# Kernel optimization log

Measured on AMD Instinct MI355X. Metric: run time of the kernel, lower is better.

## Reference

```python
import jax, jax.numpy as jnp
import numpy as np

EPS = 1e-5


def bin_act(x):
    # forward of Binaryactivation: sign (STE backward handled in fwdbwd module)
    return jnp.sign(x)


def bin_conv(x, w, stride, padding):
    # per-output-filter scaling factor = mean |w| over (in, kh, kw), detached
    scale = jax.lax.stop_gradient(jnp.mean(jnp.abs(w), axis=(1, 2, 3), keepdims=True))
    bw = scale * jnp.sign(w)
    rw = jnp.clip(w, -1.0, 1.0)
    # STE blend: forward uses binary weight, backward flows through clamp(w)
    filt = jax.lax.stop_gradient(bw - rw) + rw
    return jax.lax.conv_general_dilated(
        x, filt, window_strides=(stride, stride),
        padding=[(padding, padding), (padding, padding)],
        dimension_numbers=("NCHW", "OIHW", "NCHW"))


def batchnorm(x, gamma, beta):
    # training-mode BN: biased batch stats over (N, H, W)
    mean = jnp.mean(x, axis=(0, 2, 3), keepdims=True)
    var = jnp.mean((x - mean) ** 2, axis=(0, 2, 3), keepdims=True)
    xn = (x - mean) * jax.lax.rsqrt(var + EPS)
    return xn * gamma[None, :, None, None] + beta[None, :, None, None]


def prelu(x, a):
    a = a[None, :, None, None]
    return jnp.where(x >= 0, x, a * x)


def addbias(x, b):
    return x + b[None, :, None, None]


def setup_inputs() -> dict:
    key = jax.random.key(0)
    ks = jax.random.split(key, 4)
    C = 256
    x = jax.random.normal(ks[0], (32, C, 56, 56), dtype=jnp.float32)
    # BinaryConv weights init: uniform[0, 0.001)
    w3x3 = jax.random.uniform(ks[1], (C, C, 3, 3), dtype=jnp.float32) * 0.001
    wres = jax.random.uniform(ks[2], (C, C, 1, 1), dtype=jnp.float32) * 0.001
    zeros = jnp.zeros((C,), dtype=jnp.float32)
    ones = jnp.ones((C,), dtype=jnp.float32)
    prelu_init = jnp.full((C,), 0.25, dtype=jnp.float32)
    return {
        "x": x,
        "b1_1": zeros, "w3x3": w3x3, "bn1_g": ones, "bn1_b": zeros,
        "b1_2": zeros, "prelu1_a": prelu_init, "b1_3": zeros,
        "b2_1": zeros, "wres": wres, "bn2_g": ones, "bn2_b": zeros,
        "b2_2": zeros, "prelu2_a": prelu_init, "b2_3": zeros,
    }


def reference(x, b1_1, w3x3, bn1_g, bn1_b, b1_2, prelu1_a, b1_3,
              b2_1, wres, bn2_g, bn2_b, b2_2, prelu2_a, b2_3):
    # branch 1: bias -> sign -> binary 3x3 conv -> BN -> residual add
    x1 = bin_act(addbias(x, b1_1))
    x1 = bin_conv(x1, w3x3, stride=1, padding=1)
    x1 = batchnorm(x1, bn1_g, bn1_b)
    x = x + x1
    x = addbias(x, b1_2)
    x = prelu(x, prelu1_a)
    x = addbias(x, b1_3)
    # branch 2 (in_channel == out_channel): binary 1x1 conv residual
    x2 = bin_act(addbias(x, b2_1))
    x2 = bin_conv(x2, wres, stride=1, padding=0)
    x2 = batchnorm(x2, bn2_g, bn2_b)
    x2 = x2 + x
    x2 = addbias(x2, b2_2)
    x2 = prelu(x2, prelu2_a)
    x2 = addbias(x2, b2_3)
    return x2
```

## Files before the change

### kernel.cpp

```cpp
#include <hip/hip_runtime.h>
#include <cstdint>
#include <math.h>

#define NIMG 32
#define CCH  256
#define HH_  56
#define HW   3136
#define NPIX 100352
#define NELEM 25690112

#define OFF_PW1   0u
#define OFF_PW2   73728u
#define OFF_SC1   81920u
#define OFF_SC2   82944u
#define OFF_A1    83968u
#define OFF_B1    84992u
#define OFF_A2    86016u
#define OFF_B2    87040u
#define OFF_ST    88064u
#define ST_BYTES  524288u
#define OFF_P1    612352u
#define OFF_P2    3823616u
#define OFF_S1    7034880u
#define OFF_S2    58415104u

__global__ void prep_w_k(const float* __restrict__ w3, const float* __restrict__ wr,
                         uint32_t* __restrict__ pw1, uint32_t* __restrict__ pw2,
                         float* __restrict__ sc1, float* __restrict__ sc2) {
  const int o = blockIdx.x, l = threadIdx.x;
  const float* wo = w3 + (size_t)o * 2304;
  float s = 0.f;
  for (int i = l; i < 2304; i += 64) s += fabsf(wo[i]);
  for (int m = 32; m; m >>= 1) s += __shfl_xor(s, m, 64);
  if (l == 0) sc1[o] = s / 2304.0f;
  for (int tap = 0; tap < 9; ++tap) {
    int dh = tap / 3, dw = tap % 3;
    for (int jp = 0; jp < 4; ++jp) {
      int ci = jp * 64 + l;
      float wv = wo[(size_t)ci * 9 + dh * 3 + dw];
      unsigned long long m = __ballot(wv >= 0.0f);
      if (l == 0) {
        pw1[(size_t)(o * 9 + tap) * 8 + jp * 2 + 0] = (uint32_t)m;
        pw1[(size_t)(o * 9 + tap) * 8 + jp * 2 + 1] = (uint32_t)(m >> 32);
      }
    }
  }
  const float* wro = wr + (size_t)o * 256;
  float s2 = 0.f;
  for (int i = l; i < 256; i += 64) s2 += fabsf(wro[i]);
  for (int m = 32; m; m >>= 1) s2 += __shfl_xor(s2, m, 64);
  if (l == 0) sc2[o] = s2 / 256.0f;
  for (int jp = 0; jp < 4; ++jp) {
    unsigned long long m = __ballot(wro[jp * 64 + l] >= 0.0f);
    if (l == 0) {
      pw2[(size_t)o * 8 + jp * 2 + 0] = (uint32_t)m;
      pw2[(size_t)o * 8 + jp * 2 + 1] = (uint32_t)(m >> 32);
    }
  }
}

__global__ __launch_bounds__(256) void pack1_k(const float* __restrict__ x,
                                               const float* __restrict__ b1_1,
                                               uint32_t* __restrict__ p1) {
  const int j = blockIdx.y;
  const int pg = blockIdx.x * 256 + threadIdx.x;
  if (pg >= NPIX) return;
  const int n = pg / HW, p = pg % HW;
  const float* xb = x + (size_t)(n * CCH + j * 32) * HW + p;
  uint32_t w = 0;
#pragma unroll
  for (int cc = 0; cc < 32; ++cc) {
    float v = xb[(size_t)cc * HW] + b1_1[j * 32 + cc];
    w |= (v >= 0.0f ? 1u : 0u) << cc;
  }
  p1[(size_t)j * NPIX + pg] = w;
}

__global__ __launch_bounds__(256) void conv1_k(const uint32_t* __restrict__ p1,
                                               const uint32_t* __restrict__ pw1,
                                               short* __restrict__ S1,
                                               long long* __restrict__ st1) {
  __shared__ uint32_t act[800];
  __shared__ uint32_t wt[9216];
  const int tid = threadIdx.x;
  const int tx = blockIdx.x % 7, ty = blockIdx.x / 7;
  const int n = blockIdx.y, zh = blockIdx.z;
  const int h0 = ty * 8 - 1, w0 = tx * 8 - 1;
  for (int i = tid; i < 800; i += 256) {
    int q = i / 100, rc = i % 100;
    int r = rc / 10, cl = rc % 10;
    int hh = h0 + r, ww = w0 + cl;
    uint32_t v = 0;
    if ((unsigned)hh < 56u && (unsigned)ww < 56u)
      v = p1[(size_t)q * NPIX + (size_t)n * HW + hh * 56 + ww];
    act[rc * 8 + q] = v;
  }
  const uint32_t* pwb = pw1 + (size_t)(zh * 128) * 72;
  for (int i = tid; i < 9216; i += 256) wt[i] = pwb[i];
  __syncthreads();

  const int pxg = tid & 15, chg = tid >> 4;
  const int pr = pxg >> 1, pc4 = (pxg & 1) * 4;
  const int hg = ty * 8 + pr;
  const int wbase = tx * 8 + pc4;
  int acc[4][8];
#pragma unroll
  for (int k = 0; k < 4; ++k)
#pragma unroll
    for (int cc = 0; cc < 8; ++cc) acc[k][cc] = 0;

  for (int dh = 0; dh < 3; ++dh) {
    if ((unsigned)(hg + dh - 1) >= 56u) continue;
    const int ar = pr + dh;
    for (int dw = 0; dw < 3; ++dw) {
      const int tap = dh * 3 + dw;
#pragma unroll
      for (int q = 0; q < 2; ++q) {
        uint4 a[4];
#pragma unroll
        for (int k = 0; k < 4; ++k)
          a[k] = *(const uint4*)&act[(ar * 10 + pc4 + k + dw) * 8 + q * 4];
        uint4 wv[8];
#pragma unroll
        for (int cc = 0; cc < 8; ++cc)
          wv[cc] = *(const uint4*)&wt[((chg * 8 + cc) * 9 + tap) * 8 + q * 4];
#pragma unroll
        for (int k = 0; k < 4; ++k) {
          if ((unsigned)(wbase + k + dw - 1) < 56u) {
#pragma unroll
            for (int cc = 0; cc < 8; ++cc) {
              acc[k][cc] += __builtin_popcount(a[k].x ^ wv[cc].x) +
                            __builtin_popcount(a[k].y ^ wv[cc].y) +
                            __builtin_popcount(a[k].z ^ wv[cc].z) +
                            __builtin_popcount(a[k].w ^ wv[cc].w);
            }
          }
        }
      }
    }
  }

  const int numR = 3 - (hg == 0) - (hg == 55);
  int Vk[4];
#pragma unroll
  for (int k = 0; k < 4; ++k) {
    int wg = wbase + k;
    Vk[k] = numR * (3 - (wg == 0) - (wg == 55));
  }
  const size_t srow = (size_t)(n * CCH + zh * 128 + chg * 8) * HW + hg * 56 + wbase;
  const int slot = (blockIdx.x + 49 * (blockIdx.y + 32 * blockIdx.z)) & 63;
  unsigned long long* st = (unsigned long long*)st1;
#pragma unroll
  for (int cc = 0; cc < 8; ++cc) {
    int s[4], sm = 0, sq = 0;
#pragma unroll
    for (int k = 0; k < 4; ++k) {
      s[k] = 256 * Vk[k] - 2 * acc[k][cc];
      sm += s[k];
      sq += s[k] * s[k];
    }
    short4 o4;
    o4.x = (short)s[0]; o4.y = (short)s[1]; o4.z = (short)s[2]; o4.w = (short)s[3];
    *(short4*)&S1[srow + (size_t)cc * HW] = o4;
#pragma unroll
    for (int m = 1; m < 16; m <<= 1) {
      sm += __shfl_xor(sm, m, 64);
      sq += __shfl_xor(sq, m, 64);
    }
    if ((tid & 15) == 0) {
      int c = zh * 128 + chg * 8 + cc;
      atomicAdd(&st[(size_t)(slot * 256 + c) * 2 + 0], (unsigned long long)(long long)sm);
      atomicAdd(&st[(size_t)(slot * 256 + c) * 2 + 1], (unsigned long long)(long long)sq);
    }
  }
}

__global__ void bnfin_k(const long long* __restrict__ st, const float* __restrict__ sc,
                        const float* __restrict__ g, const float* __restrict__ b,
                        float* __restrict__ A, float* __restrict__ B) {
  const int c = threadIdx.x;
  long long sm = 0, sq = 0;
  for (int s = 0; s < 64; ++s) {
    sm += st[(size_t)(s * 256 + c) * 2 + 0];
    sq += st[(size_t)(s * 256 + c) * 2 + 1];
  }
  const double M = (double)NPIX;
  double mS = (double)sm / M;
  double vS = (double)sq / M - mS * mS;
  double scale = (double)sc[c];
  double mean = scale * mS;
  double var = scale * scale * vS;
  double rstd = 1.0 / sqrt(var + 1e-5);
  double gd = (double)g[c];
  A[c] = (float)(gd * scale * rstd);
  B[c] = (float)((double)b[c] - gd * mean * rstd);
}

__global__ __launch_bounds__(256) void pack2_k(const float* __restrict__ x,
    const short* __restrict__ S1,
    const float* __restrict__ A1, const float* __restrict__ B1,
    const float* __restrict__ b1_2, const float* __restrict__ a1,
    const float* __restrict__ b1_3, const float* __restrict__ b2_1,
    uint32_t* __restrict__ p2) {
  const int j = blockIdx.y;
  const int pg = blockIdx.x * 256 + threadIdx.x;
  if (pg >= NPIX) return;
  const int n = pg / HW, p = pg % HW;
  const size_t base = (size_t)(n * CCH + j * 32) * HW + p;
  uint32_t wd = 0;
#pragma unroll
  for (int cc = 0; cc < 32; ++cc) {
    int c = j * 32 + cc;
    size_t idx = base + (size_t)cc * HW;
    float y = A1[c] * (float)S1[idx] + B1[c];
    float u = x[idx] + y;
    u = u + b1_2[c];
    float v = u >= 0.0f ? u : a1[c] * u;
    float t = v + b1_3[c];
    wd |= ((t + b2_1[c]) >= 0.0f ? 1u : 0u) << cc;
  }
  p2[(size_t)j * NPIX + pg] = wd;
}

__global__ __launch_bounds__(256) void conv2_k(const uint32_t* __restrict__ p2,
                                               const uint32_t* __restrict__ pw2,
                                               short* __restrict__ S2,
                                               long long* __restrict__ st2) {
  __shared__ uint32_t act[512];
  __shared__ uint32_t wt[1024];
  const int tid = threadIdx.x;
  const int pg0 = blockIdx.x * 64;
  const int zh = blockIdx.y;
  for (int i = tid; i < 512; i += 256) {
    int q = i >> 6, px = i & 63;
    act[px * 8 + q] = p2[(size_t)q * NPIX + pg0 + px];
  }
  for (int i = tid; i < 1024; i += 256) wt[i] = pw2[(size_t)zh * 1024 + i];
  __syncthreads();
  const int pxg = tid & 15, chg = tid >> 4;
  int acc[4][8];
#pragma unroll
  for (int k = 0; k < 4; ++k)
#pragma unroll
    for (int cc = 0; cc < 8; ++cc) acc[k][cc] = 0;
#pragma unroll
  for (int q = 0; q < 2; ++q) {
    uint4 a[4];
#pragma unroll
    for (int k = 0; k < 4; ++k)
      a[k] = *(const uint4*)&act[(pxg * 4 + k) * 8 + q * 4];
    uint4 wv[8];
#pragma unroll
    for (int cc = 0; cc < 8; ++cc)
      wv[cc] = *(const uint4*)&wt[(chg * 8 + cc) * 8 + q * 4];
#pragma unroll
    for (int k = 0; k < 4; ++k)
#pragma unroll
      for (int cc = 0; cc < 8; ++cc)
        acc[k][cc] += __builtin_popcount(a[k].x ^ wv[cc].x) +
                      __builtin_popcount(a[k].y ^ wv[cc].y) +
                      __builtin_popcount(a[k].z ^ wv[cc].z) +
                      __builtin_popcount(a[k].w ^ wv[cc].w);
  }
  const int pg = pg0 + pxg * 4;
  const int n = pg / HW, p = pg % HW;
  const size_t srow = (size_t)(n * CCH + zh * 128 + chg * 8) * HW + p;
  const int slot = blockIdx.x & 63;
  unsigned long long* st = (unsigned long long*)st2;
#pragma unroll
  for (int cc = 0; cc < 8; ++cc) {
    int s[4], sm = 0, sq = 0;
#pragma unroll
    for (int k = 0; k < 4; ++k) {
      s[k] = 256 - 2 * acc[k][cc];
      sm += s[k];
      sq += s[k] * s[k];
    }
    short4 o4;
    o4.x = (short)s[0]; o4.y = (short)s[1]; o4.z = (short)s[2]; o4.w = (short)s[3];
    *(short4*)&S2[srow + (size_t)cc * HW] = o4;
#pragma unroll
    for (int m = 1; m < 16; m <<= 1) {
      sm += __shfl_xor(sm, m, 64);
      sq += __shfl_xor(sq, m, 64);
    }
    if ((tid & 15) == 0) {
      int c = zh * 128 + chg * 8 + cc;
      atomicAdd(&st[(size_t)(slot * 256 + c) * 2 + 0], (unsigned long long)(long long)sm);
      atomicAdd(&st[(size_t)(slot * 256 + c) * 2 + 1], (unsigned long long)(long long)sq);
    }
  }
}

__global__ __launch_bounds__(256) void final_k(const float* __restrict__ x,
    const short* __restrict__ S1, const short* __restrict__ S2,
    const float* __restrict__ A1, const float* __restrict__ B1,
    const float* __restrict__ b1_2, const float* __restrict__ a1, const float* __restrict__ b1_3,
    const float* __restrict__ A2, const float* __restrict__ B2,
    const float* __restrict__ b2_2, const float* __restrict__ a2, const float* __restrict__ b2_3,
    float* __restrict__ out) {
  const size_t i = ((size_t)blockIdx.x * 256 + threadIdx.x) * 4;
  const int c = (int)((i / HW) & 255);
  float4 xv = *(const float4*)(x + i);
  short4 s1 = *(const short4*)(S1 + i);
  short4 s2 = *(const short4*)(S2 + i);
  const float A1c = A1[c], B1c = B1[c], P12 = b1_2[c], AL1 = a1[c], P13 = b1_3[c];
  const float A2c = A2[c], B2c = B2[c], P22 = b2_2[c], AL2 = a2[c], P23 = b2_3[c];
  float xs[4] = {xv.x, xv.y, xv.z, xv.w};
  float f1[4] = {(float)s1.x, (float)s1.y, (float)s1.z, (float)s1.w};
  float f2[4] = {(float)s2.x, (float)s2.y, (float)s2.z, (float)s2.w};
  float o[4];
#pragma unroll
  for (int e = 0; e < 4; ++e) {
    float u = xs[e] + (A1c * f1[e] + B1c);
    u = u + P12;
    float v = u >= 0.0f ? u : AL1 * u;
    float t = v + P13;
    float z = (A2c * f2[e] + B2c) + t;
    z = z + P22;
    float vv = z >= 0.0f ? z : AL2 * z;
    o[e] = vv + P23;
  }
  float4 ov = {o[0], o[1], o[2], o[3]};
  *(float4*)(out + i) = ov;
}

extern "C" void kernel_launch(void* const* d_in, const int* in_sizes, int n_in,
                              void* d_out, int out_size, void* d_ws, size_t ws_size,
                              hipStream_t stream) {
  const float* x    = (const float*)d_in[0];
  const float* b1_1 = (const float*)d_in[1];
  const float* w3x3 = (const float*)d_in[2];
  const float* bn1g = (const float*)d_in[3];
  const float* bn1b = (const float*)d_in[4];
  const float* b1_2 = (const float*)d_in[5];
  const float* a1   = (const float*)d_in[6];
  const float* b1_3 = (const float*)d_in[7];
  const float* b2_1 = (const float*)d_in[8];
  const float* wres = (const float*)d_in[9];
  const float* bn2g = (const float*)d_in[10];
  const float* bn2b = (const float*)d_in[11];
  const float* b2_2 = (const float*)d_in[12];
  const float* a2   = (const float*)d_in[13];
  const float* b2_3 = (const float*)d_in[14];

  char* ws = (char*)d_ws;
  uint32_t* pw1 = (uint32_t*)(ws + OFF_PW1);
  uint32_t* pw2 = (uint32_t*)(ws + OFF_PW2);
  float* sc1 = (float*)(ws + OFF_SC1);
  float* sc2 = (float*)(ws + OFF_SC2);
  float* A1 = (float*)(ws + OFF_A1);
  float* B1 = (float*)(ws + OFF_B1);
  float* A2 = (float*)(ws + OFF_A2);
  float* B2 = (float*)(ws + OFF_B2);
  long long* st1 = (long long*)(ws + OFF_ST);
  long long* st2 = (long long*)(ws + OFF_ST + 262144u);
  uint32_t* p1 = (uint32_t*)(ws + OFF_P1);
  uint32_t* p2 = (uint32_t*)(ws + OFF_P2);
  short* S1 = (short*)(ws + OFF_S1);
  short* S2 = (short*)(ws + OFF_S2);

  hipMemsetAsync(ws + OFF_ST, 0, ST_BYTES, stream);
  prep_w_k<<<256, 64, 0, stream>>>(w3x3, wres, pw1, pw2, sc1, sc2);
  pack1_k<<<dim3(392, 8), 256, 0, stream>>>(x, b1_1, p1);
  conv1_k<<<dim3(49, 32, 2), 256, 0, stream>>>(p1, pw1, S1, st1);
  bnfin_k<<<1, 256, 0, stream>>>(st1, sc1, bn1g, bn1b, A1, B1);
  pack2_k<<<dim3(392, 8), 256, 0, stream>>>(x, S1, A1, B1, b1_2, a1, b1_3, b2_1, p2);
  conv2_k<<<dim3(1568, 2), 256, 0, stream>>>(p2, pw2, S2, st2);
  bnfin_k<<<1, 256, 0, stream>>>(st2, sc2, bn2g, bn2b, A2, B2);
  final_k<<<25088, 256, 0, stream>>>(x, S1, S2, A1, B1, b1_2, a1, b1_3,
                                     A2, B2, b2_2, a2, b2_3, (float*)d_out);
}
```

Baseline: 525.6 us.

## Restructure binary convs with border correction, tiled outputs, vectorized packing, parallel BN finalize

The 3x3 binary conv removes per-tap boundary branches. It treats zero-padding as all-ones XOR-popcount and subtracts precomputed per-filter weight-sum corrections at image borders. Each thread now computes 8 pixels by 8 channels, reusing a 10-wide activation row in registers across the three horizontal taps, and each block covers two images. Conv outputs are stored in a tile-major layout for wide stores, so pack2 and final use remapped indexing. Packing kernels process four pixels per thread with float4 loads, conv2 uses a swizzled LDS layout, and BN finalization is spread over 256 wavefronts instead of one block.

```diff
diff --git a/kernel.cpp b/kernel.cpp
--- a/kernel.cpp
+++ b/kernel.cpp
@@ -2,48 +2,59 @@
 #include <cstdint>
 #include <math.h>
 
-#define NIMG 32
-#define CCH  256
-#define HH_  56
-#define HW   3136
-#define NPIX 100352
+#define HW    3136
+#define NPIX  100352
 #define NELEM 25690112
 
 #define OFF_PW1   0u
 #define OFF_PW2   73728u
-#define OFF_SC1   81920u
-#define OFF_SC2   82944u
-#define OFF_A1    83968u
-#define OFF_B1    84992u
-#define OFF_A2    86016u
-#define OFF_B2    87040u
-#define OFF_ST    88064u
+#define OFF_CORR  81920u
+#define OFF_SC1   86016u
+#define OFF_SC2   87040u
+#define OFF_A1    88064u
+#define OFF_B1    89088u
+#define OFF_A2    90112u
+#define OFF_B2    91136u
+#define OFF_ST    92160u
 #define ST_BYTES  524288u
-#define OFF_P1    612352u
-#define OFF_P2    3823616u
-#define OFF_S1    7034880u
-#define OFF_S2    58415104u
+#define OFF_P1    616448u
+#define OFF_P2    3827712u
+#define OFF_S1    7038976u
+#define OFF_S2    58419200u
 
 __global__ void prep_w_k(const float* __restrict__ w3, const float* __restrict__ wr,
                          uint32_t* __restrict__ pw1, uint32_t* __restrict__ pw2,
-                         float* __restrict__ sc1, float* __restrict__ sc2) {
+                         float* __restrict__ sc1, float* __restrict__ sc2,
+                         short* __restrict__ corrG) {
   const int o = blockIdx.x, l = threadIdx.x;
   const float* wo = w3 + (size_t)o * 2304;
   float s = 0.f;
   for (int i = l; i < 2304; i += 64) s += fabsf(wo[i]);
   for (int m = 32; m; m >>= 1) s += __shfl_xor(s, m, 64);
   if (l == 0) sc1[o] = s / 2304.0f;
+  int wsum[9];
   for (int tap = 0; tap < 9; ++tap) {
-    int dh = tap / 3, dw = tap % 3;
+    int cnt = 0;
     for (int jp = 0; jp < 4; ++jp) {
-      int ci = jp * 64 + l;
-      float wv = wo[(size_t)ci * 9 + dh * 3 + dw];
+      float wv = wo[(size_t)(jp * 64 + l) * 9 + tap];
       unsigned long long m = __ballot(wv >= 0.0f);
+      cnt += __popcll(m);
       if (l == 0) {
         pw1[(size_t)(o * 9 + tap) * 8 + jp * 2 + 0] = (uint32_t)m;
         pw1[(size_t)(o * 9 + tap) * 8 + jp * 2 + 1] = (uint32_t)(m >> 32);
       }
     }
+    wsum[tap] = 2 * cnt - 256;
+  }
+  if (l == 0) {
+    corrG[o * 8 + 0] = (short)(wsum[0] + wsum[1] + wsum[2]);
+    corrG[o * 8 + 1] = (short)(wsum[6] + wsum[7] + wsum[8]);
+    corrG[o * 8 + 2] = (short)(wsum[0] + wsum[3] + wsum[6]);
+    corrG[o * 8 + 3] = (short)(wsum[2] + wsum[5] + wsum[8]);
+    corrG[o * 8 + 4] = (short)wsum[0];
+    corrG[o * 8 + 5] = (short)wsum[2];
+    corrG[o * 8 + 6] = (short)wsum[6];
+    corrG[o * 8 + 7] = (short)wsum[8];
   }
   const float* wro = wr + (size_t)o * 256;
   float s2 = 0.f;
@@ -63,137 +74,142 @@
                                                const float* __restrict__ b1_1,
                                                uint32_t* __restrict__ p1) {
   const int j = blockIdx.y;
-  const int pg = blockIdx.x * 256 + threadIdx.x;
-  if (pg >= NPIX) return;
-  const int n = pg / HW, p = pg % HW;
-  const float* xb = x + (size_t)(n * CCH + j * 32) * HW + p;
-  uint32_t w = 0;
+  const int gpx = blockIdx.x * 256 + threadIdx.x;
+  const int n = gpx / 784;
+  const int p4 = (gpx - n * 784) * 4;
+  const float* xb = x + ((size_t)n * 256 + j * 32) * HW + p4;
+  uint32_t w0 = 0, w1 = 0, w2 = 0, w3 = 0;
 #pragma unroll
   for (int cc = 0; cc < 32; ++cc) {
-    float v = xb[(size_t)cc * HW] + b1_1[j * 32 + cc];
-    w |= (v >= 0.0f ? 1u : 0u) << cc;
-  }
-  p1[(size_t)j * NPIX + pg] = w;
-}
-
-__global__ __launch_bounds__(256) void conv1_k(const uint32_t* __restrict__ p1,
-                                               const uint32_t* __restrict__ pw1,
-                                               short* __restrict__ S1,
-                                               long long* __restrict__ st1) {
-  __shared__ uint32_t act[800];
-  __shared__ uint32_t wt[9216];
+    float4 v = *(const float4*)(xb + (size_t)cc * HW);
+    float bb = b1_1[j * 32 + cc];
+    w0 |= (v.x + bb >= 0.f) ? (1u << cc) : 0u;
+    w1 |= (v.y + bb >= 0.f) ? (1u << cc) : 0u;
+    w2 |= (v.z + bb >= 0.f) ? (1u << cc) : 0u;
+    w3 |= (v.w + bb >= 0.f) ? (1u << cc) : 0u;
+  }
+  uint4 o = {w0, w1, w2, w3};
+  *(uint4*)&p1[(size_t)j * NPIX + gpx * 4] = o;
+}
+
+__global__ __launch_bounds__(256, 3) void conv1_k(const uint32_t* __restrict__ p1,
+    const uint32_t* __restrict__ pw1, const short* __restrict__ corrG,
+    short* __restrict__ S1, unsigned long long* __restrict__ st1) {
+  __shared__ uint32_t actS[1680];
+  __shared__ uint32_t wtS[9216];
+  __shared__ short    corrS[1024];
   const int tid = threadIdx.x;
-  const int tx = blockIdx.x % 7, ty = blockIdx.x / 7;
-  const int n = blockIdx.y, zh = blockIdx.z;
+  const int bx = blockIdx.x;
+  const int ty = bx / 7, tx = bx % 7;
+  const int by = blockIdx.y;
+  const int zh = blockIdx.z;
   const int h0 = ty * 8 - 1, w0 = tx * 8 - 1;
-  for (int i = tid; i < 800; i += 256) {
-    int q = i / 100, rc = i % 100;
-    int r = rc / 10, cl = rc % 10;
-    int hh = h0 + r, ww = w0 + cl;
+  for (int i = tid; i < 1600; i += 256) {
+    int img = i / 800, rem = i % 800;
+    int r = rem / 80, c = (rem % 80) / 8, q = i & 7;
+    int hh = h0 + r, ww = w0 + c;
     uint32_t v = 0;
     if ((unsigned)hh < 56u && (unsigned)ww < 56u)
-      v = p1[(size_t)q * NPIX + (size_t)n * HW + hh * 56 + ww];
-    act[rc * 8 + q] = v;
-  }
-  const uint32_t* pwb = pw1 + (size_t)(zh * 128) * 72;
-  for (int i = tid; i < 9216; i += 256) wt[i] = pwb[i];
+      v = p1[q * NPIX + (by * 2 + img) * HW + hh * 56 + ww];
+    actS[img * 840 + r * 84 + c * 8 + q] = v;
+  }
+  for (int i = tid; i < 2304; i += 256)
+    ((uint4*)wtS)[i] = ((const uint4*)(pw1 + (size_t)zh * 9216))[i];
+  if (tid < 128)
+    ((uint4*)corrS)[tid] = ((const uint4*)(corrG + zh * 1024))[tid];
   __syncthreads();
 
-  const int pxg = tid & 15, chg = tid >> 4;
-  const int pr = pxg >> 1, pc4 = (pxg & 1) * 4;
-  const int hg = ty * 8 + pr;
-  const int wbase = tx * 8 + pc4;
-  int acc[4][8];
-#pragma unroll
-  for (int k = 0; k < 4; ++k)
-#pragma unroll
-    for (int cc = 0; cc < 8; ++cc) acc[k][cc] = 0;
-
+  const int chg = tid & 7;
+  const int pr = (tid >> 3) & 7;
+  const int wave = tid >> 6;
+  const int img = wave >> 1;
+  const int chalf = wave & 1;
+  const int cb = chalf * 8 + chg;
+  const uint32_t* actB = actS + img * 840;
+
+  int acc[8][8];
+#pragma unroll
+  for (int j = 0; j < 8; ++j)
+#pragma unroll
+    for (int k = 0; k < 8; ++k) acc[j][k] = 0;
+
+#pragma unroll 1
   for (int dh = 0; dh < 3; ++dh) {
-    if ((unsigned)(hg + dh - 1) >= 56u) continue;
-    const int ar = pr + dh;
-    for (int dw = 0; dw < 3; ++dw) {
-      const int tap = dh * 3 + dw;
-#pragma unroll
-      for (int q = 0; q < 2; ++q) {
-        uint4 a[4];
-#pragma unroll
-        for (int k = 0; k < 4; ++k)
-          a[k] = *(const uint4*)&act[(ar * 10 + pc4 + k + dw) * 8 + q * 4];
-        uint4 wv[8];
-#pragma unroll
-        for (int cc = 0; cc < 8; ++cc)
-          wv[cc] = *(const uint4*)&wt[((chg * 8 + cc) * 9 + tap) * 8 + q * 4];
-#pragma unroll
-        for (int k = 0; k < 4; ++k) {
-          if ((unsigned)(wbase + k + dw - 1) < 56u) {
-#pragma unroll
-            for (int cc = 0; cc < 8; ++cc) {
-              acc[k][cc] += __builtin_popcount(a[k].x ^ wv[cc].x) +
-                            __builtin_popcount(a[k].y ^ wv[cc].y) +
-                            __builtin_popcount(a[k].z ^ wv[cc].z) +
-                            __builtin_popcount(a[k].w ^ wv[cc].w);
-            }
+#pragma unroll 1
+    for (int q4 = 0; q4 < 2; ++q4) {
+      uint4 a10[10];
+      const uint32_t* ar = actB + (pr + dh) * 84 + q4 * 4;
+#pragma unroll
+      for (int c2 = 0; c2 < 10; ++c2) a10[c2] = *(const uint4*)(ar + c2 * 8);
+#pragma unroll
+      for (int dw = 0; dw < 3; ++dw) {
+        const uint32_t* wr_ = wtS + cb * 72 + (dh * 3 + dw) * 8 + q4 * 4;
+#pragma unroll
+        for (int j = 0; j < 8; ++j) {
+          uint4 w = *(const uint4*)(wr_ + j * 1152);
+#pragma unroll
+          for (int k = 0; k < 8; ++k) {
+            uint4 a = a10[k + dw];
+            acc[j][k] += __builtin_popcount(a.x ^ w.x) + __builtin_popcount(a.y ^ w.y)
+                       + __builtin_popcount(a.z ^ w.z) + __builtin_popcount(a.w ^ w.w);
           }
         }
       }
     }
   }
 
-  const int numR = 3 - (hg == 0) - (hg == 55);
-  int Vk[4];
-#pragma unroll
-  for (int k = 0; k < 4; ++k) {
-    int wg = wbase + k;
-    Vk[k] = numR * (3 - (wg == 0) - (wg == 55));
-  }
-  const size_t srow = (size_t)(n * CCH + zh * 128 + chg * 8) * HW + hg * 56 + wbase;
-  const int slot = (blockIdx.x + 49 * (blockIdx.y + 32 * blockIdx.z)) & 63;
-  unsigned long long* st = (unsigned long long*)st1;
-#pragma unroll
-  for (int cc = 0; cc < 8; ++cc) {
-    int s[4], sm = 0, sq = 0;
-#pragma unroll
-    for (int k = 0; k < 4; ++k) {
-      s[k] = 256 * Vk[k] - 2 * acc[k][cc];
-      sm += s[k];
-      sq += s[k] * s[k];
-    }
-    short4 o4;
-    o4.x = (short)s[0]; o4.y = (short)s[1]; o4.z = (short)s[2]; o4.w = (short)s[3];
-    *(short4*)&S1[srow + (size_t)cc * HW] = o4;
-#pragma unroll
-    for (int m = 1; m < 16; m <<= 1) {
-      sm += __shfl_xor(sm, m, 64);
-      sq += __shfl_xor(sq, m, 64);
-    }
-    if ((tid & 15) == 0) {
-      int c = zh * 128 + chg * 8 + cc;
-      atomicAdd(&st[(size_t)(slot * 256 + c) * 2 + 0], (unsigned long long)(long long)sm);
-      atomicAdd(&st[(size_t)(slot * 256 + c) * 2 + 1], (unsigned long long)(long long)sq);
-    }
-  }
-}
-
-__global__ void bnfin_k(const long long* __restrict__ st, const float* __restrict__ sc,
+  const int n = by * 2 + img;
+  const int h = ty * 8 + pr;
+  const bool hT = (h == 0), hB = (h == 55);
+  const int slot = (bx + by * 49 + zh * 784) & 63;
+#pragma unroll
+  for (int j = 0; j < 8; ++j) {
+    const int ch_l = cb + 16 * j;
+    const short* cw = &corrS[ch_l * 8];
+    int cH = hT ? (int)cw[0] : (hB ? (int)cw[1] : 0);
+    int s[8];
+#pragma unroll
+    for (int k = 0; k < 8; ++k) s[k] = 2304 - 2 * acc[j][k] + cH;
+    if (tx == 0) s[0] += (int)cw[2] - (hT ? (int)cw[4] : (hB ? (int)cw[6] : 0));
+    if (tx == 6) s[7] += (int)cw[3] - (hT ? (int)cw[5] : (hB ? (int)cw[7] : 0));
+    int sm = 0, sq = 0;
+#pragma unroll
+    for (int k = 0; k < 8; ++k) { sm += s[k]; sq += s[k] * s[k]; }
+    uint4 val;
+    val.x = (uint32_t)(uint16_t)s[0] | ((uint32_t)(uint16_t)s[1] << 16);
+    val.y = (uint32_t)(uint16_t)s[2] | ((uint32_t)(uint16_t)s[3] << 16);
+    val.z = (uint32_t)(uint16_t)s[4] | ((uint32_t)(uint16_t)s[5] << 16);
+    val.w = (uint32_t)(uint16_t)s[6] | ((uint32_t)(uint16_t)s[7] << 16);
+    *(uint4*)&S1[(((size_t)n * 49 + bx) * 256 + zh * 128 + ch_l) * 64 + pr * 8] = val;
+#pragma unroll
+    for (int m = 8; m < 64; m <<= 1) { sm += __shfl_xor(sm, m, 64); sq += __shfl_xor(sq, m, 64); }
+    if (pr == 0) {
+      unsigned long long* st = st1 + ((size_t)(zh * 128 + ch_l) * 64 + slot) * 2;
+      atomicAdd(&st[0], (unsigned long long)(long long)sm);
+      atomicAdd(&st[1], (unsigned long long)(long long)sq);
+    }
+  }
+}
+
+__global__ void bnfin_k(const unsigned long long* __restrict__ st, const float* __restrict__ sc,
                         const float* __restrict__ g, const float* __restrict__ b,
                         float* __restrict__ A, float* __restrict__ B) {
-  const int c = threadIdx.x;
-  long long sm = 0, sq = 0;
-  for (int s = 0; s < 64; ++s) {
-    sm += st[(size_t)(s * 256 + c) * 2 + 0];
-    sq += st[(size_t)(s * 256 + c) * 2 + 1];
-  }
-  const double M = (double)NPIX;
-  double mS = (double)sm / M;
-  double vS = (double)sq / M - mS * mS;
-  double scale = (double)sc[c];
-  double mean = scale * mS;
-  double var = scale * scale * vS;
-  double rstd = 1.0 / sqrt(var + 1e-5);
-  double gd = (double)g[c];
-  A[c] = (float)(gd * scale * rstd);
-  B[c] = (float)((double)b[c] - gd * mean * rstd);
+  const int c = blockIdx.x, l = threadIdx.x;
+  long long sm = (long long)st[((size_t)c * 64 + l) * 2 + 0];
+  long long sq = (long long)st[((size_t)c * 64 + l) * 2 + 1];
+  for (int m = 1; m < 64; m <<= 1) { sm += __shfl_xor(sm, m, 64); sq += __shfl_xor(sq, m, 64); }
+  if (l == 0) {
+    const double M = (double)NPIX;
+    double mS = (double)sm / M;
+    double vS = (double)sq / M - mS * mS;
+    double scale = (double)sc[c];
+    double mean = scale * mS;
+    double var = scale * scale * vS;
+    double rstd = 1.0 / sqrt(var + 1e-5);
+    double gd = (double)g[c];
+    A[c] = (float)(gd * scale * rstd);
+    B[c] = (float)((double)b[c] - gd * mean * rstd);
+  }
 }
 
 __global__ __launch_bounds__(256) void pack2_k(const float* __restrict__ x,
@@ -203,91 +219,96 @@
     const float* __restrict__ b1_3, const float* __restrict__ b2_1,
     uint32_t* __restrict__ p2) {
   const int j = blockIdx.y;
-  const int pg = blockIdx.x * 256 + threadIdx.x;
-  if (pg >= NPIX) return;
-  const int n = pg / HW, p = pg % HW;
-  const size_t base = (size_t)(n * CCH + j * 32) * HW + p;
-  uint32_t wd = 0;
+  const int gpx = blockIdx.x * 256 + threadIdx.x;
+  const int n = gpx / 784;
+  const int p4 = (gpx - n * 784) * 4;
+  const int h = p4 / 56, w = p4 - (p4 / 56) * 56;
+  const int tile = (h >> 3) * 7 + (w >> 3);
+  const int px = (h & 7) * 8 + (w & 7);
+  const float* xb = x + ((size_t)n * 256 + j * 32) * HW + p4;
+  const short* s1b = S1 + (((size_t)n * 49 + tile) * 256 + j * 32) * 64 + px;
+  uint32_t w0 = 0, w1 = 0, w2 = 0, w3 = 0;
 #pragma unroll
   for (int cc = 0; cc < 32; ++cc) {
     int c = j * 32 + cc;
-    size_t idx = base + (size_t)cc * HW;
-    float y = A1[c] * (float)S1[idx] + B1[c];
-    float u = x[idx] + y;
-    u = u + b1_2[c];
-    float v = u >= 0.0f ? u : a1[c] * u;
-    float t = v + b1_3[c];
-    wd |= ((t + b2_1[c]) >= 0.0f ? 1u : 0u) << cc;
-  }
-  p2[(size_t)j * NPIX + pg] = wd;
+    float4 xv = *(const float4*)(xb + (size_t)cc * HW);
+    short4 s1 = *(const short4*)(s1b + cc * 64);
+    float Ac = A1[c], Bc = B1[c], p12 = b1_2[c], al = a1[c], p13 = b1_3[c], p21 = b2_1[c];
+    float u, v, t;
+    u = xv.x + (Ac * (float)s1.x + Bc) + p12; v = u >= 0.f ? u : al * u; t = v + p13 + p21;
+    w0 |= (t >= 0.f) ? (1u << cc) : 0u;
+    u = xv.y + (Ac * (float)s1.y + Bc) + p12; v = u >= 0.f ? u : al * u; t = v + p13 + p21;
+    w1 |= (t >= 0.f) ? (1u << cc) : 0u;
+    u = xv.z + (Ac * (float)s1.z + Bc) + p12; v = u >= 0.f ? u : al * u; t = v + p13 + p21;
+    w2 |= (t >= 0.f) ? (1u << cc) : 0u;
+    u = xv.w + (Ac * (float)s1.w + Bc) + p12; v = u >= 0.f ? u : al * u; t = v + p13 + p21;
+    w3 |= (t >= 0.f) ? (1u << cc) : 0u;
+  }
+  uint4 o = {w0, w1, w2, w3};
+  *(uint4*)&p2[(size_t)j * NPIX + gpx * 4] = o;
 }
 
 __global__ __launch_bounds__(256) void conv2_k(const uint32_t* __restrict__ p2,
                                                const uint32_t* __restrict__ pw2,
                                                short* __restrict__ S2,
-                                               long long* __restrict__ st2) {
-  __shared__ uint32_t act[512];
-  __shared__ uint32_t wt[1024];
+                                               unsigned long long* __restrict__ st2) {
+  __shared__ uint32_t actS[512];
+  __shared__ uint32_t wtS[1024];
   const int tid = threadIdx.x;
-  const int pg0 = blockIdx.x * 64;
+  const int bx = blockIdx.x;
   const int zh = blockIdx.y;
+  const int pg0 = bx * 64;
   for (int i = tid; i < 512; i += 256) {
-    int q = i >> 6, px = i & 63;
-    act[px * 8 + q] = p2[(size_t)q * NPIX + pg0 + px];
-  }
-  for (int i = tid; i < 1024; i += 256) wt[i] = pw2[(size_t)zh * 1024 + i];
+    int gq = i >> 2, ws_ = i & 3;
+    int pxl = gq >> 1, q4 = gq & 1;
+    int q = q4 * 4 + ws_;
+    actS[((gq ^ ((gq >> 3) & 15)) << 2) + ws_] = p2[q * NPIX + pg0 + pxl];
+  }
+  if (tid < 256)
+    ((uint4*)wtS)[tid] = ((const uint4*)(pw2 + zh * 1024))[tid];
   __syncthreads();
   const int pxg = tid & 15, chg = tid >> 4;
-  int acc[4][8];
-#pragma unroll
-  for (int k = 0; k < 4; ++k)
-#pragma unroll
-    for (int cc = 0; cc < 8; ++cc) acc[k][cc] = 0;
-#pragma unroll
-  for (int q = 0; q < 2; ++q) {
+  int acc[8][4];
+#pragma unroll
+  for (int j = 0; j < 8; ++j)
+#pragma unroll
+    for (int k = 0; k < 4; ++k) acc[j][k] = 0;
+#pragma unroll
+  for (int q4 = 0; q4 < 2; ++q4) {
     uint4 a[4];
 #pragma unroll
-    for (int k = 0; k < 4; ++k)
-      a[k] = *(const uint4*)&act[(pxg * 4 + k) * 8 + q * 4];
-    uint4 wv[8];
-#pragma unroll
-    for (int cc = 0; cc < 8; ++cc)
-      wv[cc] = *(const uint4*)&wt[(chg * 8 + cc) * 8 + q * 4];
-#pragma unroll
-    for (int k = 0; k < 4; ++k)
-#pragma unroll
-      for (int cc = 0; cc < 8; ++cc)
-        acc[k][cc] += __builtin_popcount(a[k].x ^ wv[cc].x) +
-                      __builtin_popcount(a[k].y ^ wv[cc].y) +
-                      __builtin_popcount(a[k].z ^ wv[cc].z) +
-                      __builtin_popcount(a[k].w ^ wv[cc].w);
-  }
-  const int pg = pg0 + pxg * 4;
-  const int n = pg / HW, p = pg % HW;
-  const size_t srow = (size_t)(n * CCH + zh * 128 + chg * 8) * HW + p;
-  const int slot = blockIdx.x & 63;
-  unsigned long long* st = (unsigned long long*)st2;
-#pragma unroll
-  for (int cc = 0; cc < 8; ++cc) {
+    for (int k = 0; k < 4; ++k) {
+      int gq = 8 * pxg + 2 * k + q4;
+      a[k] = *(const uint4*)&actS[(gq ^ pxg) << 2];
+    }
+#pragma unroll
+    for (int j = 0; j < 8; ++j) {
+      uint4 w = *(const uint4*)&wtS[(chg + 16 * j) * 8 + q4 * 4];
+#pragma unroll
+      for (int k = 0; k < 4; ++k)
+        acc[j][k] += __builtin_popcount(a[k].x ^ w.x) + __builtin_popcount(a[k].y ^ w.y)
+                   + __builtin_popcount(a[k].z ^ w.z) + __builtin_popcount(a[k].w ^ w.w);
+    }
+  }
+  const int slot = bx & 63;
+#pragma unroll
+  for (int j = 0; j < 8; ++j) {
+    const int c_l = chg + 16 * j;
     int s[4], sm = 0, sq = 0;
 #pragma unroll
     for (int k = 0; k < 4; ++k) {
-      s[k] = 256 - 2 * acc[k][cc];
-      sm += s[k];
-      sq += s[k] * s[k];
+      s[k] = 256 - 2 * acc[j][k];
+      sm += s[k]; sq += s[k] * s[k];
     }
     short4 o4;
     o4.x = (short)s[0]; o4.y = (short)s[1]; o4.z = (short)s[2]; o4.w = (short)s[3];
-    *(short4*)&S2[srow + (size_t)cc * HW] = o4;
-#pragma unroll
-    for (int m = 1; m < 16; m <<= 1) {
-      sm += __shfl_xor(sm, m, 64);
-      sq += __shfl_xor(sq, m, 64);
-    }
-    if ((tid & 15) == 0) {
-      int c = zh * 128 + chg * 8 + cc;
-      atomicAdd(&st[(size_t)(slot * 256 + c) * 2 + 0], (unsigned long long)(long long)sm);
-      atomicAdd(&st[(size_t)(slot * 256 + c) * 2 + 1], (unsigned long long)(long long)sq);
+    *(short4*)&S2[(((size_t)bx * 256) + zh * 128 + c_l) * 64 + pxg * 4] = o4;
+#pragma unroll
+    for (int m = 1; m < 16; m <<= 1) { sm += __shfl_xor(sm, m, 64); sq += __shfl_xor(sq, m, 64); }
+    if (pxg == 0) {
+      unsigned long long* st = st2 + ((size_t)(zh * 128 + c_l) * 64 + slot) * 2;
+      atomicAdd(&st[0], (unsigned long long)(long long)sm);
+      atomicAdd(&st[1], (unsigned long long)(long long)sq);
     }
   }
 }
@@ -299,11 +320,18 @@
     const float* __restrict__ A2, const float* __restrict__ B2,
     const float* __restrict__ b2_2, const float* __restrict__ a2, const float* __restrict__ b2_3,
     float* __restrict__ out) {
-  const size_t i = ((size_t)blockIdx.x * 256 + threadIdx.x) * 4;
-  const int c = (int)((i / HW) & 255);
-  float4 xv = *(const float4*)(x + i);
-  short4 s1 = *(const short4*)(S1 + i);
-  short4 s2 = *(const short4*)(S2 + i);
+  const int gi = blockIdx.x * 256 + threadIdx.x;
+  const int i4 = gi * 4;
+  const int nc = i4 / 3136;
+  const int p = i4 - nc * 3136;
+  const int n = nc >> 8, c = nc & 255;
+  const int h = p / 56, w = p - (p / 56) * 56;
+  const int tile = (h >> 3) * 7 + (w >> 3);
+  const int px = (h & 7) * 8 + (w & 7);
+  short4 s1 = *(const short4*)&S1[(((size_t)n * 49 + tile) * 256 + c) * 64 + px];
+  const int pg = n * 3136 + p;
+  short4 s2 = *(const short4*)&S2[((size_t)(pg >> 6) * 256 + c) * 64 + (pg & 63)];
+  float4 xv = *(const float4*)&x[i4];
   const float A1c = A1[c], B1c = B1[c], P12 = b1_2[c], AL1 = a1[c], P13 = b1_3[c];
   const float A2c = A2[c], B2c = B2[c], P22 = b2_2[c], AL2 = a2[c], P23 = b2_3[c];
   float xs[4] = {xv.x, xv.y, xv.z, xv.w};
@@ -322,7 +350,7 @@
     o[e] = vv + P23;
   }
   float4 ov = {o[0], o[1], o[2], o[3]};
-  *(float4*)(out + i) = ov;
+  *(float4*)&out[i4] = ov;
 }
 
 extern "C" void kernel_launch(void* const* d_in, const int* in_sizes, int n_in,
@@ -347,27 +375,28 @@
   char* ws = (char*)d_ws;
   uint32_t* pw1 = (uint32_t*)(ws + OFF_PW1);
   uint32_t* pw2 = (uint32_t*)(ws + OFF_PW2);
+  short* corrG = (short*)(ws + OFF_CORR);
   float* sc1 = (float*)(ws + OFF_SC1);
   float* sc2 = (float*)(ws + OFF_SC2);
   float* A1 = (float*)(ws + OFF_A1);
   float* B1 = (float*)(ws + OFF_B1);
   float* A2 = (float*)(ws + OFF_A2);
   float* B2 = (float*)(ws + OFF_B2);
-  long long* st1 = (long long*)(ws + OFF_ST);
-  long long* st2 = (long long*)(ws + OFF_ST + 262144u);
+  unsigned long long* st1 = (unsigned long long*)(ws + OFF_ST);
+  unsigned long long* st2 = (unsigned long long*)(ws + OFF_ST + 262144u);
   uint32_t* p1 = (uint32_t*)(ws + OFF_P1);
   uint32_t* p2 = (uint32_t*)(ws + OFF_P2);
   short* S1 = (short*)(ws + OFF_S1);
   short* S2 = (short*)(ws + OFF_S2);
 
   hipMemsetAsync(ws + OFF_ST, 0, ST_BYTES, stream);
-  prep_w_k<<<256, 64, 0, stream>>>(w3x3, wres, pw1, pw2, sc1, sc2);
-  pack1_k<<<dim3(392, 8), 256, 0, stream>>>(x, b1_1, p1);
-  conv1_k<<<dim3(49, 32, 2), 256, 0, stream>>>(p1, pw1, S1, st1);
-  bnfin_k<<<1, 256, 0, stream>>>(st1, sc1, bn1g, bn1b, A1, B1);
-  pack2_k<<<dim3(392, 8), 256, 0, stream>>>(x, S1, A1, B1, b1_2, a1, b1_3, b2_1, p2);
+  prep_w_k<<<256, 64, 0, stream>>>(w3x3, wres, pw1, pw2, sc1, sc2, corrG);
+  pack1_k<<<dim3(98, 8), 256, 0, stream>>>(x, b1_1, p1);
+  conv1_k<<<dim3(49, 16, 2), 256, 0, stream>>>(p1, pw1, corrG, S1, st1);
+  bnfin_k<<<256, 64, 0, stream>>>(st1, sc1, bn1g, bn1b, A1, B1);
+  pack2_k<<<dim3(98, 8), 256, 0, stream>>>(x, S1, A1, B1, b1_2, a1, b1_3, b2_1, p2);
   conv2_k<<<dim3(1568, 2), 256, 0, stream>>>(p2, pw2, S2, st2);
-  bnfin_k<<<1, 256, 0, stream>>>(st2, sc2, bn2g, bn2b, A2, B2);
+  bnfin_k<<<256, 64, 0, stream>>>(st2, sc2, bn2g, bn2b, A2, B2);
   final_k<<<25088, 256, 0, stream>>>(x, S1, S2, A1, B1, b1_2, a1, b1_3,
                                      A2, B2, b2_2, a2, b2_3, (float*)d_out);
 }
```

Measured after the change: 508.5 us. 1.03x faster.
